# Performance work log

Hardware: AMD Instinct MI355X
Metric: run time of the kernel (lower is better)

The kernel has to match this reference:

```python
import jax, jax.numpy as jnp
import numpy as np

B, N, DIM, HEADS, DH = 2, 1024, 1024, 16, 64
SEQ_LEN, MEM_NUM = 1024, 4
EH, EW, ET = 4, 4, 1  # mem_expand_size
PH, PW = 4, 4        # patch grid
CUR_PATCH_IDX = 5
MEM_IDXS = [0, 1, 4, 5]


def _locate(idx):
    # get_pos_from_idx_down_right
    num_frame = PH * PW
    inner = idx % num_frame
    return (inner % PH, inner // PH, idx // num_frame)


def _rel_idxs():
    rph, rpw = 2 * EH + 1, 2 * EW + 1
    frame = rph * rpw
    src = _locate(CUR_PATCH_IDX)
    out = []
    for t in MEM_IDXS + [CUR_PATCH_IDX]:
        tg = _locate(t)
        out.append((tg[0] - src[0] + EH) * rpw + (tg[1] - src[1] + EW) + (tg[2] - src[2] + ET) * frame)
    return np.array(out, np.int32)


def setup_inputs() -> dict:
    key = jax.random.key(0)
    ks = jax.random.split(key, 8)
    inner = HEADS * DH
    s = 0.02
    return {
        "x": jax.random.normal(ks[0], (B, N, DIM), jnp.float32),
        "mem": jax.random.normal(ks[1], (B, MEM_NUM * SEQ_LEN, DIM), jnp.float32),
        "mask": jnp.zeros((B, MEM_NUM * SEQ_LEN + N), bool),
        "rel_idxs": jnp.asarray(_rel_idxs()),
        "Wq": jax.random.normal(ks[2], (DIM, inner), jnp.float32) * s,
        "Wk": jax.random.normal(ks[3], (DIM, inner), jnp.float32) * s,
        "Wv": jax.random.normal(ks[4], (DIM, inner), jnp.float32) * s,
        "Wo": jax.random.normal(ks[5], (inner, DIM), jnp.float32) * s,
        "bo": jnp.zeros((DIM,), jnp.float32),
        "rel_table": jax.random.normal(ks[6], ((2 * EH + 1) * (2 * EW + 1) * (2 * ET + 1), HEADS), jnp.float32) * s,
    }


def reference(x, mem, mask, rel_idxs, Wq, Wk, Wv, Wo, bo, rel_table):
    b, n, dim = x.shape
    heads = rel_table.shape[1]
    dh = Wq.shape[1] // heads
    mem_num = rel_idxs.shape[0] - 1
    mem_len = mem.shape[1]
    seq_len = mem_len // mem_num
    scale = dh ** (-0.5)

    kx = jnp.concatenate([mem, x], axis=1)           # [b, j, dim]
    j = kx.shape[1]
    q = (x @ Wq).reshape(b, n, heads, dh).transpose(0, 2, 1, 3)   # bhid
    k = (kx @ Wk).reshape(b, j, heads, dh).transpose(0, 2, 1, 3)  # bhjd
    v = (kx @ Wv).reshape(b, j, heads, dh).transpose(0, 2, 1, 3)

    # relative position bias: a per-head scalar added to every K feature
    rel_emb = rel_table[rel_idxs].T                  # [h, mem_num+1]
    bias_mem = jnp.repeat(rel_emb[:, :mem_num], seq_len, axis=1)  # [h, mem_len]
    bias_cur = jnp.broadcast_to(rel_emb[:, -1:], (heads, j - mem_len))
    bias = jnp.concatenate([bias_mem, bias_cur], axis=1)          # [h, j]
    k = k + bias[None, :, :, None]

    dots = jnp.einsum('bhid,bhjd->bhij', q, k) * scale
    neg = -jnp.finfo(dots.dtype).max
    dots = jnp.where(mask[:, None, None, :], neg, dots)
    causal = jnp.triu(jnp.ones((n, j), bool), j - n + 1)
    dots = jnp.where(causal, neg, dots)

    attn = jax.nn.softmax(dots, axis=-1)
    out = jnp.einsum('bhij,bhjd->bhid', attn, v)
    out = out.transpose(0, 2, 1, 3).reshape(b, n, heads * dh) @ Wo + bo
    new_mem = x[:, -seq_len:]
    return out, new_mem
```

## Files before the change

### kernel.cpp

```cpp
#include <hip/hip_runtime.h>
#include <float.h>

#define NQ    1024
#define JTOT  5120
#define MEML  4096
#define SCL2  0.18033688011112042f

typedef __attribute__((ext_vector_type(8))) short bf16x8;
typedef __attribute__((ext_vector_type(8))) unsigned short ush8;
typedef __attribute__((ext_vector_type(4))) unsigned short ush4;
typedef __attribute__((ext_vector_type(4))) float f32x4;

static __device__ __forceinline__ unsigned short f2bf(float x) {
    union { float f; unsigned u; } v; v.f = x;
    unsigned r = (v.u + 0x7fffu + ((v.u >> 16) & 1u)) >> 16;
    return (unsigned short)r;
}
static __device__ __forceinline__ unsigned pack2(float f0, float f1) {
    union { float f; unsigned u; } a, b; a.f = f1; b.f = f0;
    return __builtin_amdgcn_perm(a.u, b.u, 0x07060302u);
}

static __device__ __forceinline__ void gld16(const void* g, void* l) {
    __builtin_amdgcn_global_load_lds(
        (const __attribute__((address_space(1))) unsigned int*)g,
        (__attribute__((address_space(3))) unsigned int*)l, 16, 0, 0);
}

__global__ __launch_bounds__(256)
void prep_kernel(const float* __restrict__ x, const float* __restrict__ mem,
                 const unsigned char* __restrict__ mask,
                 const float* __restrict__ W0, const float* __restrict__ W1,
                 const float* __restrict__ W2, const float* __restrict__ W3,
                 unsigned short* __restrict__ xb, unsigned short* __restrict__ memb,
                 unsigned short* __restrict__ wt, float* __restrict__ mbp)
{
    __shared__ float Ts[32][33];
    const int bid = blockIdx.x;
    const int t   = threadIdx.x;
    if (bid < 5120) {
        const float* src = (bid < 1024) ? x : mem;
        unsigned short* dst = (bid < 1024) ? xb : memb;
        const size_t i = (size_t)((bid < 1024) ? bid : bid - 1024) * 2048 + t * 8;
        float4 a = *(const float4*)(src + i);
        float4 b = *(const float4*)(src + i + 4);
        ush8 o;
        o[0] = f2bf(a.x); o[1] = f2bf(a.y); o[2] = f2bf(a.z); o[3] = f2bf(a.w);
        o[4] = f2bf(b.x); o[5] = f2bf(b.y); o[6] = f2bf(b.z); o[7] = f2bf(b.w);
        *(ush8*)(dst + i) = o;
    } else if (bid < 5160) {
        const int i = (bid - 5120) * 256 + t;
        mbp[i] = mask[i] ? -1.0e30f : 0.0f;
    } else {
        const int idx = bid - 5160;
        const int z   = idx >> 10;
        const int rem = idx & 1023;
        const float* W = (z == 0) ? W0 : (z == 1) ? W1 : (z == 2) ? W2 : W3;
        unsigned short* D = wt + (size_t)z * 1024 * 1024;
        const int n0 = (rem & 31) * 32, k0 = (rem >> 5) * 32;
        const int tr = t >> 3, tc = (t & 7) * 4;
        float4 v = *(const float4*)(W + (size_t)(k0 + tr) * 1024 + n0 + tc);
        Ts[tr][tc + 0] = v.x; Ts[tr][tc + 1] = v.y;
        Ts[tr][tc + 2] = v.z; Ts[tr][tc + 3] = v.w;
        __syncthreads();
        ush4 o;
        o[0] = f2bf(Ts[tc + 0][tr]); o[1] = f2bf(Ts[tc + 1][tr]);
        o[2] = f2bf(Ts[tc + 2][tr]); o[3] = f2bf(Ts[tc + 3][tr]);
        *(ush4*)(D + (size_t)(n0 + tr) * 1024 + k0 + tc) = o;
    }
}

__global__ __launch_bounds__(256)
void mgemm01_kernel(const unsigned short* __restrict__ xb,
                    const unsigned short* __restrict__ memb,
                    const unsigned short* __restrict__ wt,
                    unsigned short* __restrict__ Qb, unsigned short* __restrict__ Kb,
                    unsigned short* __restrict__ Vb,
                    const float* __restrict__ rel_table, const int* __restrict__ rel_idxs)
{
    __shared__ unsigned short Al[128 * 64];
    __shared__ unsigned short Bl[128 * 64];

    const int t    = threadIdx.x;
    const int lane = t & 63;
    const int w    = t >> 6;
    const int wr   = w >> 1, wc = w & 1;
    const int l15  = lane & 15;
    const int quad = lane >> 4;
    const int l7   = l15 & 7;

    const int bid = blockIdx.x;
    int mode, bx, by;
    if (bid < 384) {
        mode = 0;
        const int c = bid & 7, i = bid >> 3;
        bx = 3 * c + i % 3;
        by = i / 3;
    } else {
        mode = 1;
        const int p = bid - 384;
        const int c = p & 7, i = p >> 3;
        const int half = i >> 6;
        const int j    = i & 63;
        bx = half * 8 + (j & 7);
        by = 8 * c + (j >> 3);
    }
    const int mat = bx >> 3;
    const int n0  = (bx & 7) * 128;
    const int m0  = by * 128;
    const unsigned short* A = (mode == 0) ? xb : memb;
    const unsigned short* B = wt + (size_t)((mode == 0) ? mat : mat + 1) * 1024 * 1024;

    f32x4 acc[4][4];
    #pragma unroll
    for (int i = 0; i < 4; i++)
        #pragma unroll
        for (int j = 0; j < 4; j++) acc[i][j] = (f32x4){0.f, 0.f, 0.f, 0.f};

    for (int k0 = 0; k0 < 1024; k0 += 64) {
        __syncthreads();
        #pragma unroll
        for (int it = 0; it < 4; it++) {
            const int lin  = it * 256 + t;
            const int row  = lin >> 3;
            const int colb = ((lin & 7) ^ (row & 7)) * 8;
            unsigned short* albase = &Al[(size_t)(it * 256 + w * 64) * 8];
            unsigned short* blbase = &Bl[(size_t)(it * 256 + w * 64) * 8];
            gld16(A + (size_t)(m0 + row) * 1024 + k0 + colb, albase);
            gld16(B + (size_t)(n0 + row) * 1024 + k0 + colb, blbase);
        }
        __syncthreads();
        bf16x8 af[4][2], bfr[4][2];
        #pragma unroll
        for (int i = 0; i < 4; i++) {
            const int R = wr * 64 + i * 16 + l15;
            af[i][0] = *(const bf16x8*)&Al[R * 64 + ((quad ^ l7) << 3)];
            af[i][1] = *(const bf16x8*)&Al[R * 64 + (((4 | quad) ^ l7) << 3)];
        }
        #pragma unroll
        for (int j = 0; j < 4; j++) {
            const int R = wc * 64 + j * 16 + l15;
            bfr[j][0] = *(const bf16x8*)&Bl[R * 64 + ((quad ^ l7) << 3)];
            bfr[j][1] = *(const bf16x8*)&Bl[R * 64 + (((4 | quad) ^ l7) << 3)];
        }
        __builtin_amdgcn_s_setprio(1);
        #pragma unroll
        for (int i = 0; i < 4; i++)
            #pragma unroll
            for (int j = 0; j < 4; j++) {
                acc[i][j] = __builtin_amdgcn_mfma_f32_16x16x32_bf16(af[i][0], bfr[j][0], acc[i][j], 0, 0, 0);
                acc[i][j] = __builtin_amdgcn_mfma_f32_16x16x32_bf16(af[i][1], bfr[j][1], acc[i][j], 0, 0, 0);
            }
        __builtin_amdgcn_s_setprio(0);
    }

    const bool isQ = (mode == 0) && (mat == 0);
    const bool isK = (mode == 0) ? (mat == 1) : (mat == 0);
    if (!isQ && !isK) {
        #pragma unroll
        for (int i = 0; i < 4; i++) {
            const int r0 = m0 + wr * 64 + i * 16 + quad * 4;
            const int bb = (mode == 0) ? (r0 >> 10) : (r0 >> 12);
            const int j0 = (mode == 0) ? 4096 + (r0 & 1023) : (r0 & 4095);
            #pragma unroll
            for (int jb = 0; jb < 4; jb++) {
                const int col = n0 + wc * 64 + jb * 16 + l15;
                ush4 o;
                o[0] = f2bf(acc[i][jb][0]); o[1] = f2bf(acc[i][jb][1]);
                o[2] = f2bf(acc[i][jb][2]); o[3] = f2bf(acc[i][jb][3]);
                *(ush4*)(Vb + ((size_t)((bb * 16 + (col >> 6)) * 64 + (col & 63))) * JTOT + j0) = o;
            }
        }
    } else {
        #pragma unroll
        for (int i = 0; i < 4; i++)
            #pragma unroll
            for (int reg = 0; reg < 4; reg++) {
                const int r = m0 + wr * 64 + i * 16 + quad * 4 + reg;
                int bb, idx, chunk;
                if (mode == 0) { bb = r >> 10; idx = isK ? 4096 + (r & 1023) : (r & 1023); chunk = 4; }
                else           { bb = r >> 12; idx = r & 4095; chunk = idx >> 10; }
                #pragma unroll
                for (int jb = 0; jb < 4; jb++) {
                    const int col = n0 + wc * 64 + jb * 16 + l15;
                    const int hh = col >> 6, dh = col & 63;
                    float v = acc[i][jb][reg];
                    if (isK) {
                        v += rel_table[rel_idxs[chunk] * 16 + hh];
                        Kb[((size_t)(bb * 16 + hh) * JTOT + idx) * 64 + dh] = f2bf(v);
                    } else {
                        Qb[((size_t)(bb * 16 + hh) * NQ + idx) * 64 + dh] = f2bf(v);
                    }
                }
            }
    }
}

__global__ __launch_bounds__(256)
void mgemm2_kernel(const unsigned short* __restrict__ A,
                   const unsigned short* __restrict__ WT,
                   float* __restrict__ outF, const float* __restrict__ bo,
                   const float* __restrict__ x, float* __restrict__ newmem)
{
    __shared__ unsigned short Al[64 * 64];
    __shared__ unsigned short Bl[128 * 64];

    const int t = threadIdx.x;
    if (blockIdx.z == 1) {
        const int blk = blockIdx.y * 8 + blockIdx.x;
        const size_t base = (size_t)blk * 8192 + t * 4;
        #pragma unroll
        for (int i = 0; i < 8; i++)
            *(float4*)(newmem + base + (size_t)i * 1024) =
                *(const float4*)(x + base + (size_t)i * 1024);
        return;
    }

    const int lane = t & 63;
    const int w    = t >> 6;
    const int l15  = lane & 15;
    const int quad = lane >> 4;
    const int l7   = l15 & 7;
    const int n0   = blockIdx.x * 128;
    const int m0   = blockIdx.y * 64;

    f32x4 acc[4][2];
    #pragma unroll
    for (int i = 0; i < 4; i++)
        #pragma unroll
        for (int j = 0; j < 2; j++) acc[i][j] = (f32x4){0.f, 0.f, 0.f, 0.f};

    for (int k0 = 0; k0 < 1024; k0 += 64) {
        __syncthreads();
        #pragma unroll
        for (int it = 0; it < 2; it++) {
            const int lin  = it * 256 + t;
            const int row  = lin >> 3;
            const int colb = ((lin & 7) ^ (row & 7)) * 8;
            gld16(A + (size_t)(m0 + row) * 1024 + k0 + colb,
                  &Al[(size_t)(it * 256 + w * 64) * 8]);
        }
        #pragma unroll
        for (int it = 0; it < 4; it++) {
            const int lin  = it * 256 + t;
            const int row  = lin >> 3;
            const int colb = ((lin & 7) ^ (row & 7)) * 8;
            gld16(WT + (size_t)(n0 + row) * 1024 + k0 + colb,
                  &Bl[(size_t)(it * 256 + w * 64) * 8]);
        }
        __syncthreads();
        bf16x8 af[4][2], bfr[2][2];
        #pragma unroll
        for (int i = 0; i < 4; i++) {
            const int R = i * 16 + l15;
            af[i][0] = *(const bf16x8*)&Al[R * 64 + ((quad ^ l7) << 3)];
            af[i][1] = *(const bf16x8*)&Al[R * 64 + (((4 | quad) ^ l7) << 3)];
        }
        #pragma unroll
        for (int j = 0; j < 2; j++) {
            const int R = w * 32 + j * 16 + l15;
            bfr[j][0] = *(const bf16x8*)&Bl[R * 64 + ((quad ^ l7) << 3)];
            bfr[j][1] = *(const bf16x8*)&Bl[R * 64 + (((4 | quad) ^ l7) << 3)];
        }
        #pragma unroll
        for (int i = 0; i < 4; i++)
            #pragma unroll
            for (int j = 0; j < 2; j++) {
                acc[i][j] = __builtin_amdgcn_mfma_f32_16x16x32_bf16(af[i][0], bfr[j][0], acc[i][j], 0, 0, 0);
                acc[i][j] = __builtin_amdgcn_mfma_f32_16x16x32_bf16(af[i][1], bfr[j][1], acc[i][j], 0, 0, 0);
            }
    }

    #pragma unroll
    for (int i = 0; i < 4; i++)
        #pragma unroll
        for (int reg = 0; reg < 4; reg++) {
            const int r = m0 + i * 16 + quad * 4 + reg;
            #pragma unroll
            for (int j = 0; j < 2; j++) {
                const int col = n0 + w * 32 + j * 16 + l15;
                outF[(size_t)r * 1024 + col] = acc[i][j][reg] + bo[col];
            }
        }
}

__global__ __launch_bounds__(256)
void attn6_kernel(const unsigned short* __restrict__ qh,
                  const unsigned short* __restrict__ kh,
                  const unsigned short* __restrict__ vt,
                  const float* __restrict__ mb,
                  unsigned short* __restrict__ ao)
{
    __shared__ unsigned short Ks[128 * 64];
    __shared__ unsigned short Vs[64 * 128];
    __shared__ unsigned short Ps[64 * 128];
    __shared__ float Ls[4][64];

    const int t    = threadIdx.x;
    const int lane = t & 63;
    const int w    = t >> 6;
    const int l15  = lane & 15;
    const int quad = lane >> 4;
    const int l7   = l15 & 7;

    const int flat = blockIdx.x + 16 * blockIdx.y + 256 * blockIdx.z;
    const int xcd  = flat & 7;
    const int idx  = flat >> 3;
    const int qt   = idx >> 2;
    const int hb   = (xcd << 2) | (idx & 3);
    const int h    = hb & 15;
    const int b    = hb >> 4;

    const int qbase = qt * 64;
    const int qg    = qbase + w * 16 + l15;

    bf16x8 bq0[4], bq1[4];
    #pragma unroll
    for (int qb = 0; qb < 4; qb++) {
        const unsigned short* qrow =
            qh + (((size_t)(b * 16 + h) * NQ + qbase + qb * 16 + l15) << 6);
        bq0[qb] = *(const bf16x8*)(qrow + quad * 8);
        bq1[qb] = *(const bf16x8*)(qrow + 32 + quad * 8);
    }

    const int krow = t >> 3;
    const int kcol = (t & 7) * 8;
    const int ksw  = ((t & 7) ^ (krow & 7)) * 8;
    const int vrow = t >> 4;
    const int vu   = t & 15;
    const int vcol = vu * 8;
    const int vsw  = ((vu & 8) | ((vu ^ (vrow & 7)) & 7)) * 8;

    const unsigned short* kbase = kh + (((size_t)(b * 16 + h) * JTOT) << 6);
    const unsigned short* vbase = vt + (((size_t)(b * 16 + h)) << 6) * JTOT;
    const float* mbb = mb + b * JTOT;

    f32x4 oa[4];
    #pragma unroll
    for (int mt = 0; mt < 4; mt++) oa[mt] = (f32x4){0.f, 0.f, 0.f, 0.f};
    float lacc[4] = {0.f, 0.f, 0.f, 0.f};

    const int ntp = (qt + 66) >> 1;

    ush8 kst[4], vst[4];
    #pragma unroll
    for (int p = 0; p < 4; p++)
        kst[p] = *(const ush8*)(kbase + ((size_t)(krow + 32 * p) << 6) + kcol);
    #pragma unroll
    for (int p = 0; p < 4; p++)
        vst[p] = *(const ush8*)(vbase + (size_t)(vrow + 16 * p) * JTOT + vcol);

    const int prow = (w * 16 + l15) * 128;

    for (int jt = 0; jt < ntp; jt++) {
        const int jbase = jt * 128;
        __syncthreads();
        #pragma unroll
        for (int p = 0; p < 4; p++)
            *(ush8*)&Ks[(krow + 32 * p) * 64 + ksw] = kst[p];
        #pragma unroll
        for (int p = 0; p < 4; p++)
            *(ush8*)&Vs[(vrow + 16 * p) * 128 + vsw] = vst[p];
        __syncthreads();

        if (jt + 1 < ntp) {
            const int jb2 = jbase + 128;
            #pragma unroll
            for (int p = 0; p < 4; p++)
                kst[p] = *(const ush8*)(kbase + ((size_t)(jb2 + krow + 32 * p) << 6) + kcol);
            #pragma unroll
            for (int p = 0; p < 4; p++)
                vst[p] = *(const ush8*)(vbase + (size_t)(vrow + 16 * p) * JTOT + jb2 + vcol);
        }

        f32x4 sa[2][4];
        __builtin_amdgcn_s_setprio(1);
        #pragma unroll
        for (int kk = 0; kk < 2; kk++) {
            const int mt2 = 2 * w + kk;
            const int ra  = (mt2 * 16 + l15) * 64;
            const bf16x8 ak0 = *(const bf16x8*)&Ks[ra + ((quad ^ l7) << 3)];
            const bf16x8 ak1 = *(const bf16x8*)&Ks[ra + (((4 | quad) ^ l7) << 3)];
            #pragma unroll
            for (int qb = 0; qb < 4; qb++) {
                f32x4 s = (f32x4){0.f, 0.f, 0.f, 0.f};
                s = __builtin_amdgcn_mfma_f32_16x16x32_bf16(ak0, bq0[qb], s, 0, 0, 0);
                s = __builtin_amdgcn_mfma_f32_16x16x32_bf16(ak1, bq1[qb], s, 0, 0, 0);
                sa[kk][qb] = s;
            }
        }
        __builtin_amdgcn_s_setprio(0);

        #pragma unroll
        for (int kk = 0; kk < 2; kk++) {
            const float4 mv = *(const float4*)(mbb + jbase + (2 * w + kk) * 16 + quad * 4);
            #pragma unroll
            for (int qb = 0; qb < 4; qb++) {
                sa[kk][qb][0] = sa[kk][qb][0] * SCL2 + mv.x;
                sa[kk][qb][1] = sa[kk][qb][1] * SCL2 + mv.y;
                sa[kk][qb][2] = sa[kk][qb][2] * SCL2 + mv.z;
                sa[kk][qb][3] = sa[kk][qb][3] * SCL2 + mv.w;
            }
        }
        if (jt == ntp - 1) {
            #pragma unroll
            for (int qb = 0; qb < 4; qb++) {
                const int tl = qbase + qb * 16 + l15 + 4096 - jbase;
                #pragma unroll
                for (int kk = 0; kk < 2; kk++)
                    #pragma unroll
                    for (int r = 0; r < 4; r++)
                        if ((2 * w + kk) * 16 + quad * 4 + r > tl) sa[kk][qb][r] = -1.0e30f;
            }
        }

        #pragma unroll
        for (int kk = 0; kk < 2; kk++)
            #pragma unroll
            for (int qb = 0; qb < 4; qb++)
                #pragma unroll
                for (int r = 0; r < 4; r++) {
                    const float pv = __builtin_amdgcn_exp2f(sa[kk][qb][r]);
                    sa[kk][qb][r] = pv;
                    lacc[qb] += pv;
                }

        #pragma unroll
        for (int kk = 0; kk < 2; kk++) {
            const int u  = 4 * w + 2 * kk + (quad >> 1);
            const int up = (u & 8) | ((u ^ l7) & 7);
            #pragma unroll
            for (int qb = 0; qb < 4; qb++) {
                uint2 pk;
                pk.x = pack2(sa[kk][qb][0], sa[kk][qb][1]);
                pk.y = pack2(sa[kk][qb][2], sa[kk][qb][3]);
                *(uint2*)&Ps[(qb * 16 + l15) * 128 + up * 8 + (quad & 1) * 4] = pk;
            }
        }
        __syncthreads();

        __builtin_amdgcn_s_setprio(1);
        #pragma unroll
        for (int s = 0; s < 4; s++) {
            const int u  = quad + 4 * s;
            const int up = (u & 8) | ((u ^ l7) & 7);
            const bf16x8 bp = *(const bf16x8*)&Ps[prow + up * 8];
            #pragma unroll
            for (int mt = 0; mt < 4; mt++) {
                const bf16x8 av = *(const bf16x8*)&Vs[(mt * 16 + l15) * 128 + up * 8];
                oa[mt] = __builtin_amdgcn_mfma_f32_16x16x32_bf16(av, bp, oa[mt], 0, 0, 0);
            }
        }
        __builtin_amdgcn_s_setprio(0);
    }

    #pragma unroll
    for (int qb = 0; qb < 4; qb++) {
        lacc[qb] += __shfl_xor(lacc[qb], 16);
        lacc[qb] += __shfl_xor(lacc[qb], 32);
    }
    if (quad == 0) {
        #pragma unroll
        for (int qb = 0; qb < 4; qb++) Ls[w][qb * 16 + l15] = lacc[qb];
    }
    __syncthreads();
    const float l = Ls[0][w * 16 + l15] + Ls[1][w * 16 + l15] +
                    Ls[2][w * 16 + l15] + Ls[3][w * 16 + l15];
    const float inv = 1.0f / l;
    unsigned short* arow = ao + ((size_t)(b * NQ + qg)) * 1024 + h * 64;
    #pragma unroll
    for (int mt = 0; mt < 4; mt++) {
        ush4 o;
        o[0] = f2bf(oa[mt][0] * inv); o[1] = f2bf(oa[mt][1] * inv);
        o[2] = f2bf(oa[mt][2] * inv); o[3] = f2bf(oa[mt][3] * inv);
        *(ush4*)(arow + mt * 16 + quad * 4) = o;
    }
}

extern "C" void kernel_launch(void* const* d_in, const int* in_sizes, int n_in,
                              void* d_out, int out_size, void* d_ws, size_t ws_size,
                              hipStream_t stream)
{
    const float* x        = (const float*)d_in[0];
    const float* mem      = (const float*)d_in[1];
    const unsigned char* mask = (const unsigned char*)d_in[2];
    const int*   rel_idxs = (const int*)d_in[3];
    const float* Wq       = (const float*)d_in[4];
    const float* Wk       = (const float*)d_in[5];
    const float* Wv       = (const float*)d_in[6];
    const float* Wo       = (const float*)d_in[7];
    const float* bo       = (const float*)d_in[8];
    const float* rel_table= (const float*)d_in[9];

    float* out = (float*)d_out;
    const size_t M1 = (size_t)1024 * 1024;
    unsigned short* xb   = (unsigned short*)d_ws;
    unsigned short* memb = xb   + 2 * M1;
    unsigned short* wt   = memb + 8 * M1;
    unsigned short* qb   = wt   + 4 * M1;
    unsigned short* kb   = qb   + 2 * M1;
    unsigned short* vb   = kb   + 10 * M1;
    unsigned short* aob  = vb   + 10 * M1;
    float* mbp = (float*)(aob + 2 * M1);

    prep_kernel<<<9256, 256, 0, stream>>>(
        x, mem, mask, Wq, Wk, Wv, Wo, xb, memb, wt, mbp);
    mgemm01_kernel<<<1408, 256, 0, stream>>>(
        xb, memb, wt, qb, kb, vb, rel_table, rel_idxs);
    attn6_kernel<<<dim3(16, 16, 2), 256, 0, stream>>>(qb, kb, vb, mbp, aob);
    mgemm2_kernel<<<dim3(8, 32, 2), 256, 0, stream>>>(
        aob, wt + 3 * M1, out, bo, x, out + (size_t)2048 * 1024);
}
```

Baseline: 294.6 us.

## Double-buffer LDS tiles in projection GEMM to overlap loads with MFMA

Splits the shared-memory A/B tiles into two ping-pong buffers so the global-to-LDS loads for the next K slice are issued while the MFMAs run on the current one. This halves the barriers per K step and is meant to hide global load latency in the QKV projection kernel. It doubles LDS use to 64KB per block, which can lower occupancy, and it drops the s_setprio hints around the MFMA loop.

```diff
diff --git a/kernel.cpp b/kernel.cpp
--- a/kernel.cpp
+++ b/kernel.cpp
@@ -78,8 +78,8 @@
                     unsigned short* __restrict__ Vb,
                     const float* __restrict__ rel_table, const int* __restrict__ rel_idxs)
 {
-    __shared__ unsigned short Al[128 * 64];
-    __shared__ unsigned short Bl[128 * 64];
+    __shared__ unsigned short Al0[128 * 64], Bl0[128 * 64];
+    __shared__ unsigned short Al1[128 * 64], Bl1[128 * 64];
 
     const int t    = threadIdx.x;
     const int lane = t & 63;
@@ -111,39 +111,39 @@
     const unsigned short* A = (mode == 0) ? xb : memb;
     const unsigned short* B = wt + (size_t)((mode == 0) ? mat : mat + 1) * 1024 * 1024;
 
-    f32x4 acc[4][4];
-    #pragma unroll
-    for (int i = 0; i < 4; i++)
-        #pragma unroll
-        for (int j = 0; j < 4; j++) acc[i][j] = (f32x4){0.f, 0.f, 0.f, 0.f};
-
-    for (int k0 = 0; k0 < 1024; k0 += 64) {
-        __syncthreads();
+    auto stage = [&](unsigned short* Ad, unsigned short* Bd, int k0) {
         #pragma unroll
         for (int it = 0; it < 4; it++) {
             const int lin  = it * 256 + t;
             const int row  = lin >> 3;
             const int colb = ((lin & 7) ^ (row & 7)) * 8;
-            unsigned short* albase = &Al[(size_t)(it * 256 + w * 64) * 8];
-            unsigned short* blbase = &Bl[(size_t)(it * 256 + w * 64) * 8];
-            gld16(A + (size_t)(m0 + row) * 1024 + k0 + colb, albase);
-            gld16(B + (size_t)(n0 + row) * 1024 + k0 + colb, blbase);
-        }
-        __syncthreads();
+            gld16(A + (size_t)(m0 + row) * 1024 + k0 + colb,
+                  Ad + (size_t)(it * 256 + w * 64) * 8);
+            gld16(B + (size_t)(n0 + row) * 1024 + k0 + colb,
+                  Bd + (size_t)(it * 256 + w * 64) * 8);
+        }
+    };
+
+    f32x4 acc[4][4];
+    #pragma unroll
+    for (int i = 0; i < 4; i++)
+        #pragma unroll
+        for (int j = 0; j < 4; j++) acc[i][j] = (f32x4){0.f, 0.f, 0.f, 0.f};
+
+    auto compute = [&](const unsigned short* As, const unsigned short* Bs) {
         bf16x8 af[4][2], bfr[4][2];
         #pragma unroll
         for (int i = 0; i < 4; i++) {
             const int R = wr * 64 + i * 16 + l15;
-            af[i][0] = *(const bf16x8*)&Al[R * 64 + ((quad ^ l7) << 3)];
-            af[i][1] = *(const bf16x8*)&Al[R * 64 + (((4 | quad) ^ l7) << 3)];
+            af[i][0] = *(const bf16x8*)&As[R * 64 + ((quad ^ l7) << 3)];
+            af[i][1] = *(const bf16x8*)&As[R * 64 + (((4 | quad) ^ l7) << 3)];
         }
         #pragma unroll
         for (int j = 0; j < 4; j++) {
             const int R = wc * 64 + j * 16 + l15;
-            bfr[j][0] = *(const bf16x8*)&Bl[R * 64 + ((quad ^ l7) << 3)];
-            bfr[j][1] = *(const bf16x8*)&Bl[R * 64 + (((4 | quad) ^ l7) << 3)];
-        }
-        __builtin_amdgcn_s_setprio(1);
+            bfr[j][0] = *(const bf16x8*)&Bs[R * 64 + ((quad ^ l7) << 3)];
+            bfr[j][1] = *(const bf16x8*)&Bs[R * 64 + (((4 | quad) ^ l7) << 3)];
+        }
         #pragma unroll
         for (int i = 0; i < 4; i++)
             #pragma unroll
@@ -151,8 +151,22 @@
                 acc[i][j] = __builtin_amdgcn_mfma_f32_16x16x32_bf16(af[i][0], bfr[j][0], acc[i][j], 0, 0, 0);
                 acc[i][j] = __builtin_amdgcn_mfma_f32_16x16x32_bf16(af[i][1], bfr[j][1], acc[i][j], 0, 0, 0);
             }
-        __builtin_amdgcn_s_setprio(0);
-    }
+    };
+
+    stage(Al0, Bl0, 0);
+    __syncthreads();
+    for (int e = 0; e < 14; e += 2) {
+        stage(Al1, Bl1, (e + 1) << 6);
+        compute(Al0, Bl0);
+        __syncthreads();
+        stage(Al0, Bl0, (e + 2) << 6);
+        compute(Al1, Bl1);
+        __syncthreads();
+    }
+    stage(Al1, Bl1, 15 << 6);
+    compute(Al0, Bl0);
+    __syncthreads();
+    compute(Al1, Bl1);
 
     const bool isQ = (mode == 0) && (mat == 0);
     const bool isK = (mode == 0) ? (mat == 1) : (mat == 0);
```

Measured after the change: 278.7 us. -5.4%, faster.
